# Performance work log

Hardware: AMD Instinct MI355X
Metric: run time of the kernel (lower is better)

The kernel has to match this reference:

```python
import jax, jax.numpy as jnp
import numpy as np

B, T, C, H, WINDOW = 256, 1024, 128, 256, 24


def setup_inputs() -> dict:
    key = jax.random.key(0)
    ks = jax.random.split(key, 9)
    s = 1.0 / np.sqrt(H)  # torch LSTMCell uniform init scale
    return {
        "x": jax.random.normal(ks[0], (B, T, C), dtype=jnp.float32),
        "W_ih": jax.random.uniform(ks[1], (4 * H, C), jnp.float32, -s, s),
        "W_hh": jax.random.uniform(ks[2], (4 * H, H), jnp.float32, -s, s),
        "b_ih": jax.random.uniform(ks[3], (4 * H,), jnp.float32, -s, s),
        "b_hh": jax.random.uniform(ks[4], (4 * H,), jnp.float32, -s, s),
        "W_skip": jax.random.normal(ks[5], (H, H), dtype=jnp.float32) * np.sqrt(2.0 / (H + H)),
        "b_skip": jnp.zeros((H,), jnp.float32),
        "h0": jax.random.normal(ks[6], (1, H), dtype=jnp.float32) * np.sqrt(2.0 / (1 + H)),
        "c0": jax.random.normal(ks[7], (1, H), dtype=jnp.float32) * np.sqrt(2.0 / (1 + H)),
    }


def reference(x, W_ih, W_hh, b_ih, b_hh, W_skip, b_skip, h0, c0):
    Bb, Tt, _ = x.shape
    Hh = h0.shape[1]
    h = jnp.tile(h0, (Bb, 1))
    c = jnp.tile(c0, (Bb, 1))
    # ring buffer of the last WINDOW hidden states (output[i-WINDOW] lives at slot i % WINDOW)
    buf = jnp.zeros((WINDOW, Bb, Hh), x.dtype)
    # precompute the input contribution to the gates for all timesteps: [T, B, 4H]
    xg = jnp.einsum('btc,gc->tbg', x, W_ih) + b_ih + b_hh

    def step(carry, inp):
        h, c, buf = carry
        xg_t, i = inp
        idx = i % WINDOW
        skip = jax.lax.dynamic_index_in_dim(buf, idx, 0, keepdims=False)  # output[i-WINDOW]
        mask = (i >= WINDOW).astype(x.dtype)
        h_in = h + mask * (skip @ W_skip.T + b_skip)
        gates = xg_t + h_in @ W_hh.T  # [B, 4H]
        gi, gf, gg, go = jnp.split(gates, 4, axis=-1)  # torch order: i, f, g, o
        c_new = jax.nn.sigmoid(gf) * c + jax.nn.sigmoid(gi) * jnp.tanh(gg)
        h_new = jax.nn.sigmoid(go) * jnp.tanh(c_new)
        buf = jax.lax.dynamic_update_index_in_dim(buf, h_new, idx, 0)
        return (h_new, c_new, buf), h_new

    (h, c, _), out = jax.lax.scan(step, (h, c, buf), (xg, jnp.arange(Tt)))
    output = jnp.swapaxes(out, 0, 1)  # [B, T, H]
    return output, h, c
```

## Files before the change

### kernel.cpp

```cpp
#include <hip/hip_runtime.h>
#include <cstddef>

#define Bn  256
#define Tn  1024
#define Cn  128
#define Hn  256
#define WIN 24

#define NRG 16
#define NUG 8
#define RPB 16
#define UPB 32

#define AGENT __HIP_MEMORY_SCOPE_AGENT
#define RLX   __ATOMIC_RELAXED

typedef __attribute__((ext_vector_type(8))) short bf16x8;
typedef __attribute__((ext_vector_type(4))) float f32x4;

#define MFMA(a, b, c) __builtin_amdgcn_mfma_f32_16x16x32_bf16((a), (b), (c), 0, 0, 0)

struct __align__(64) Flag { int v; int pad[15]; };
__device__ Flag g_flag[NRG][NUG];
__device__ unsigned short g_hx_hi[2][Bn][Hn];
__device__ unsigned short g_hx_lo[2][Bn][Hn];

__device__ inline unsigned short f2bf(float f) {
    union { float f; unsigned u; } v; v.f = f;
    unsigned r = (v.u + 0x7FFF + ((v.u >> 16) & 1)) >> 16;
    return (unsigned short)r;
}
__device__ inline float bf2f(unsigned short b) {
    union { unsigned u; float f; } v; v.u = (unsigned)b << 16;
    return v.f;
}
__device__ inline void split8(const float* s, bf16x8& hi, bf16x8& lo) {
    #pragma unroll
    for (int e = 0; e < 8; ++e) {
        unsigned short h = f2bf(s[e]);
        float r = s[e] - bf2f(h);
        hi[e] = (short)h;
        lo[e] = (short)f2bf(r);
    }
}
__device__ inline float fsigm(float x) {
    return __builtin_amdgcn_rcpf(1.f + exp2f(x * -1.442695041f));
}
__device__ inline float ftanh(float x) {
    return 1.f - 2.f * __builtin_amdgcn_rcpf(1.f + exp2f(x * 2.885390082f));
}

__global__ __launch_bounds__(256) void init_sync(const float* __restrict__ h0) {
    int i = blockIdx.x * 256 + threadIdx.x;
    int b = i >> 8, u = i & 255;
    float hv = h0[u];
    unsigned short hi = f2bf(hv);
    g_hx_hi[0][b][u] = hi;
    g_hx_lo[0][b][u] = f2bf(hv - bf2f(hi));
    g_hx_hi[1][b][u] = 0;
    g_hx_lo[1][b][u] = 0;
    if (i < NRG * NUG) ((Flag*)g_flag)[i].v = 0;
}

__global__ __launch_bounds__(512, 1) void lstm_persist(
    const float* __restrict__ x,
    const float* __restrict__ W_ih, const float* __restrict__ W_hh,
    const float* __restrict__ b_ih, const float* __restrict__ b_hh,
    const float* __restrict__ W_skip, const float* __restrict__ b_skip,
    const float* __restrict__ h0, const float* __restrict__ c0,
    float* __restrict__ outp, float* __restrict__ hbuf, float* __restrict__ cbuf)
{
    __shared__ bf16x8 s_ga[2][12][64];
    __shared__ bf16x8 s_sa[2][8][64];
    __shared__ float  s_part[8][64][4];
    __shared__ float  s_sk[4][2][64][4];
    __shared__ __align__(16) unsigned short s_hown_hi[16][32];
    __shared__ __align__(16) unsigned short s_hown_lo[16][32];
    __shared__ float  s_hout[16][32];
    __shared__ float  s_bias[128];
    __shared__ float  s_bskip[UPB];
    __shared__ float  s_pad[5000];

    const int tid = threadIdx.x;
    if (tid == 0) ((volatile float*)s_pad)[0] = 0.f;

    const int xcd = blockIdx.x & 7, slot = blockIdx.x >> 3;
    const int rg = (xcd << 1) | (slot >> 3), ug = slot & 7;
    const int row0 = rg * RPB, u0 = ug * UPB;

    const int w = tid >> 6, lane = tid & 63;
    const int g  = w >> 1, uh = w & 1;
    const int nl = lane & 15, kq = lane >> 4;
    const int sm = lane & 15;
    const int k0 = w * 32 + kq * 8;
    const bool own = (w == ug);
    const int cm = tid >> 5, cu = tid & 31;
    const int cli = ((cm >> 2) << 4) | (cu & 15), cr = cm & 3, cuh = cu >> 4;
    const int ksx2 = w - 4;
    const int mx2 = lane & 15, kqx2 = lane >> 4;

    bf16x8 whh_hi[8], whh_lo[8], wx_hi[4], wx_lo[4], ws_hi[2], ws_lo[2];
    {
        const int Rg = g * Hn + u0 + uh * 16 + nl;
        const float* wr = W_hh + (size_t)Rg * Hn;
        #pragma unroll
        for (int j = 0; j < 8; ++j) {
            float tmp[8];
            const int k = j * 32 + kq * 8;
            #pragma unroll
            for (int e = 0; e < 8; ++e) tmp[e] = wr[k + e];
            split8(tmp, whh_hi[j], whh_lo[j]);
        }
        const float* wr2 = W_ih + (size_t)Rg * Cn;
        #pragma unroll
        for (int j = 0; j < 4; ++j) {
            float tmp[8];
            const int k = j * 32 + kq * 8;
            #pragma unroll
            for (int e = 0; e < 8; ++e) tmp[e] = wr2[k + e];
            split8(tmp, wx_hi[j], wx_lo[j]);
        }
        const int Rs = u0 + uh * 16 + nl;
        const float* wr3 = W_skip + (size_t)Rs * Hn;
        #pragma unroll
        for (int j = 0; j < 2; ++j) {
            float tmp[8];
            const int k = ((w >> 1) * 2 + j) * 32 + kq * 8;
            #pragma unroll
            for (int e = 0; e < 8; ++e) tmp[e] = wr3[k + e];
            split8(tmp, ws_hi[j], ws_lo[j]);
        }
    }
    if (tid < 128) s_bias[tid] = b_ih[(tid >> 5) * Hn + u0 + (tid & 31)]
                               + b_hh[(tid >> 5) * Hn + u0 + (tid & 31)];
    if (tid < UPB) s_bskip[tid] = b_skip[u0 + tid];

    float c_reg = c0[u0 + cu];
    {
        float hv = h0[u0 + cu];
        unsigned short phi = f2bf(hv);
        s_hown_hi[cm][cu] = phi;
        s_hown_lo[cm][cu] = f2bf(hv - bf2f(phi));
    }
    if (tid < 256) {
        const int ksx = tid >> 6;
        const float* src = x + (size_t)(row0 + sm) * (Tn * Cn) + ksx * 32 + kq * 8;
        float tmp[8];
        #pragma unroll
        for (int e = 0; e < 8; ++e) tmp[e] = src[e];
        bf16x8 hi, lo; split8(tmp, hi, lo);
        s_ga[0][ksx][lane] = hi; s_ga[1][ksx][lane] = lo;
    }
    f32x4 ring_a = {0.f,0.f,0.f,0.f}, ring_b = {0.f,0.f,0.f,0.f};
    __syncthreads();

    for (int t = 0; t < Tn; ++t) {
        const bool do_ring = (t >= WIN - 1) && (t < Tn - 1);
        const bool nr      = (t >= WIN - 2) && (t < Tn - 2);
        const int  par     = t & 1;

        int fv = 0x7fffffff;
        if (!own) fv = __hip_atomic_load(&g_flag[rg][w].v, RLX, AGENT);

        if (do_ring) {
            asm volatile("s_waitcnt vmcnt(0)" : "+v"(ring_a), "+v"(ring_b) :: "memory");
            float rvv[8];
            #pragma unroll
            for (int e = 0; e < 4; ++e) { rvv[e] = ring_a[e]; rvv[4 + e] = ring_b[e]; }
            bf16x8 hi, lo; split8(rvv, hi, lo);
            s_sa[0][w][lane] = hi; s_sa[1][w][lane] = lo;
        }
        __syncthreads();

        const unsigned short* hip_ = &g_hx_hi[par][row0 + sm][k0];
        const unsigned short* lop_ = &g_hx_lo[par][row0 + sm][k0];
        bf16x8 ha, hb;
        bool have = false;
        if (!own && fv >= t) {
            have = true;
            asm volatile("global_load_dwordx4 %0, %2, off sc0 sc1\n\t"
                         "global_load_dwordx4 %1, %3, off sc0 sc1"
                         : "=&v"(ha), "=&v"(hb) : "v"(hip_), "v"(lop_) : "memory");
        }

        f32x4 ac0 = {0.f,0.f,0.f,0.f}, ac1 = {0.f,0.f,0.f,0.f}, ac2 = {0.f,0.f,0.f,0.f};
        #pragma unroll
        for (int j = 0; j < 4; ++j) {
            bf16x8 ah = s_ga[0][j][lane], al = s_ga[1][j][lane];
            ac0 = MFMA(ah, wx_hi[j], ac0);
            ac1 = MFMA(ah, wx_lo[j], ac1);
            ac2 = MFMA(al, wx_hi[j], ac2);
        }
        if (do_ring) {
            f32x4 sk0 = {0.f,0.f,0.f,0.f}, sk1 = {0.f,0.f,0.f,0.f}, sk2 = {0.f,0.f,0.f,0.f};
            #pragma unroll
            for (int j = 0; j < 2; ++j) {
                const int ks = (w >> 1) * 2 + j;
                bf16x8 ah = s_sa[0][ks][lane], al = s_sa[1][ks][lane];
                sk0 = MFMA(ah, ws_hi[j], sk0);
                sk1 = MFMA(ah, ws_lo[j], sk1);
                sk2 = MFMA(al, ws_hi[j], sk2);
            }
            *(f32x4*)&s_sk[w >> 1][w & 1][lane][0] = sk0 + sk1 + sk2;
        }
        if (!own && !have) {
            fv = __hip_atomic_load(&g_flag[rg][w].v, RLX, AGENT);
            if (fv >= t) {
                have = true;
                asm volatile("global_load_dwordx4 %0, %2, off sc0 sc1\n\t"
                             "global_load_dwordx4 %1, %3, off sc0 sc1"
                             : "=&v"(ha), "=&v"(hb) : "v"(hip_), "v"(lop_) : "memory");
            }
        }

        if (!own) {
            while (fv < t)
                fv = __hip_atomic_load(&g_flag[rg][w].v, RLX, AGENT);
            if (!have) {
                asm volatile("global_load_dwordx4 %0, %2, off sc0 sc1\n\t"
                             "global_load_dwordx4 %1, %3, off sc0 sc1"
                             : "=&v"(ha), "=&v"(hb) : "v"(hip_), "v"(lop_) : "memory");
            }
            asm volatile("s_waitcnt vmcnt(0)" : "+v"(ha), "+v"(hb) :: "memory");
            s_ga[0][4 + w][lane] = ha;
            s_ga[1][4 + w][lane] = hb;
        } else {
            s_ga[0][4 + w][lane] = *(const bf16x8*)&s_hown_hi[sm][kq * 8];
            s_ga[1][4 + w][lane] = *(const bf16x8*)&s_hown_lo[sm][kq * 8];
        }
        f32x4 xa, xb;
        const bool xst = (w >= 4) && (t + 1 < Tn);
        if (xst) {
            const float* xsrc = x + (size_t)(row0 + mx2) * (Tn * Cn)
                                  + (size_t)(t + 1) * Cn + ksx2 * 32 + kqx2 * 8;
            xa = *(const f32x4*)xsrc;
            xb = *(const f32x4*)(xsrc + 4);
        }
        __syncthreads();

        #pragma unroll
        for (int j = 0; j < 8; ++j) {
            bf16x8 ah = s_ga[0][4 + j][lane], al = s_ga[1][4 + j][lane];
            ac0 = MFMA(ah, whh_hi[j], ac0);
            ac1 = MFMA(ah, whh_lo[j], ac1);
            ac2 = MFMA(al, whh_hi[j], ac2);
        }
        *(f32x4*)&s_part[w][lane][0] = ac0 + ac1 + ac2;
        __syncthreads();

        {
            float gv[4];
            #pragma unroll
            for (int g2 = 0; g2 < 4; ++g2)
                gv[g2] = s_part[g2 * 2 + cuh][cli][cr] + s_bias[g2 * 32 + cu];
            float si = fsigm(gv[0]);
            float sf = fsigm(gv[1]);
            float gt = ftanh(gv[2]);
            float so = fsigm(gv[3]);
            c_reg = sf * c_reg + si * gt;
            float hn = so * ftanh(c_reg);
            s_hout[cm][cu] = hn;
            if (t < Tn - 1) {
                float hin = hn;
                if (do_ring) {
                    float sk = s_sk[0][cuh][cli][cr] + s_sk[1][cuh][cli][cr]
                             + s_sk[2][cuh][cli][cr] + s_sk[3][cuh][cli][cr];
                    hin += sk + s_bskip[cu];
                }
                unsigned short phi = f2bf(hin);
                s_hown_hi[cm][cu] = phi;
                s_hown_lo[cm][cu] = f2bf(hin - bf2f(phi));
            } else {
                hbuf[(size_t)(row0 + cm) * Hn + u0 + cu] = hn;
                cbuf[(size_t)(row0 + cm) * Hn + u0 + cu] = c_reg;
            }
        }
        __syncthreads();

        if (tid < 64) {
            if (t < Tn - 1) {
                const int r8 = tid >> 2, q = tid & 3;
                f32x4 v = *(const f32x4*)&s_hown_hi[r8][q * 8];
                unsigned short* dst = &g_hx_hi[par ^ 1][row0 + r8][u0 + q * 8];
                asm volatile("global_store_dwordx4 %0, %1, off sc0 sc1"
                             :: "v"(dst), "v"(v) : "memory");
            }
        } else if (tid < 128) {
            if (t < Tn - 1) {
                const int r8 = (tid - 64) >> 2, q = tid & 3;
                f32x4 v = *(const f32x4*)&s_hown_lo[r8][q * 8];
                unsigned short* dst = &g_hx_lo[par ^ 1][row0 + r8][u0 + q * 8];
                asm volatile("global_store_dwordx4 %0, %1, off sc0 sc1"
                             :: "v"(dst), "v"(v) : "memory");
            }
        } else if (tid < 256) {
            const int i = tid - 128, r8 = i >> 3, q = i & 7;
            f32x4 v = *(const f32x4*)&s_hout[r8][q * 4];
            float* dst = &outp[(size_t)(row0 + r8) * (Tn * Hn) + (size_t)t * Hn + u0 + q * 4];
            asm volatile("global_store_dwordx4 %0, %1, off sc0 sc1"
                         :: "v"(dst), "v"(v) : "memory");
        } else if (xst) {
            float tmp[8];
            #pragma unroll
            for (int e = 0; e < 4; ++e) { tmp[e] = xa[e]; tmp[4 + e] = xb[e]; }
            bf16x8 hi, lo; split8(tmp, hi, lo);
            s_ga[0][ksx2][lane] = hi;
            s_ga[1][ksx2][lane] = lo;
        }

        asm volatile("s_waitcnt vmcnt(0)" ::: "memory");
        __syncthreads();
        if (t < Tn - 1 && tid == 0)
            __hip_atomic_store(&g_flag[rg][ug].v, t + 1, RLX, AGENT);

        if (nr) {
            const float* rsrc = outp + (size_t)(row0 + sm) * (Tn * Hn)
                                     + (size_t)(t - (WIN - 2)) * Hn + k0;
            asm volatile("global_load_dwordx4 %0, %2, off sc0 sc1\n\t"
                         "global_load_dwordx4 %1, %2, off offset:16 sc0 sc1"
                         : "=&v"(ring_a), "=&v"(ring_b) : "v"(rsrc) : "memory");
        }
    }
}

extern "C" void kernel_launch(void* const* d_in, const int* in_sizes, int n_in,
                              void* d_out, int out_size, void* d_ws, size_t ws_size,
                              hipStream_t stream)
{
    const float* x      = (const float*)d_in[0];
    const float* W_ih   = (const float*)d_in[1];
    const float* W_hh   = (const float*)d_in[2];
    const float* b_ih   = (const float*)d_in[3];
    const float* b_hh   = (const float*)d_in[4];
    const float* W_skip = (const float*)d_in[5];
    const float* b_skip = (const float*)d_in[6];
    const float* h0     = (const float*)d_in[7];
    const float* c0     = (const float*)d_in[8];

    float* outp = (float*)d_out;
    float* hbuf = outp + (size_t)Bn * Tn * Hn;
    float* cbuf = hbuf + (size_t)Bn * Hn;

    init_sync<<<256, 256, 0, stream>>>(h0);
    lstm_persist<<<128, 512, 0, stream>>>(x, W_ih, W_hh, b_ih, b_hh,
                                          W_skip, b_skip, h0, c0, outp, hbuf, cbuf);
}
```

Before: 3.184 ms.

## Publish per-wave ready flags and prefetch flag loads to shorten the cross-block handshake

Each producer wave now publishes its own flag (one for the hi half, one for the lo half) right after its stores drain. This replaces the block-wide waitcnt, __syncthreads and single-thread flag store at the end of each step. Consumers prefetch both flags with one dwordx2 load issued at the end of the previous step and take their minimum. The ring-buffer conversion and skip MFMAs move after the W_hh MFMAs, so the per-step critical path through the inter-block dependency gets shorter. The change drops one barrier per step but relies on per-wave waitcnt ordering and relaxed atomics for memory visibility.

```diff
diff --git a/kernel.cpp b/kernel.cpp
--- a/kernel.cpp
+++ b/kernel.cpp
@@ -17,11 +17,12 @@
 
 typedef __attribute__((ext_vector_type(8))) short bf16x8;
 typedef __attribute__((ext_vector_type(4))) float f32x4;
+typedef __attribute__((ext_vector_type(2))) int   i32x2;
 
 #define MFMA(a, b, c) __builtin_amdgcn_mfma_f32_16x16x32_bf16((a), (b), (c), 0, 0, 0)
 
-struct __align__(64) Flag { int v; int pad[15]; };
-__device__ Flag g_flag[NRG][NUG];
+struct __align__(64) Flag2 { int f0; int f1; int pad[14]; };
+__device__ Flag2 g_flag[NRG][NUG];
 __device__ unsigned short g_hx_hi[2][Bn][Hn];
 __device__ unsigned short g_hx_lo[2][Bn][Hn];
 
@@ -59,7 +60,7 @@
     g_hx_lo[0][b][u] = f2bf(hv - bf2f(hi));
     g_hx_hi[1][b][u] = 0;
     g_hx_lo[1][b][u] = 0;
-    if (i < NRG * NUG) ((Flag*)g_flag)[i].v = 0;
+    if (i < NRG * NUG * 16) ((int*)g_flag)[i] = 0;
 }
 
 __global__ __launch_bounds__(512, 1) void lstm_persist(
@@ -152,35 +153,33 @@
         s_ga[0][ksx][lane] = hi; s_ga[1][ksx][lane] = lo;
     }
     f32x4 ring_a = {0.f,0.f,0.f,0.f}, ring_b = {0.f,0.f,0.f,0.f};
-    __syncthreads();
+    i32x2 fs = {0, 0};
+    const int* fp2 = &g_flag[rg][w].f0;
+    if (!own)
+        asm volatile("global_load_dwordx2 %0, %1, off sc0 sc1"
+                     : "=&v"(fs) : "v"(fp2) : "memory");
 
     for (int t = 0; t < Tn; ++t) {
         const bool do_ring = (t >= WIN - 1) && (t < Tn - 1);
         const bool nr      = (t >= WIN - 2) && (t < Tn - 2);
         const int  par     = t & 1;
 
-        int fv = 0x7fffffff;
-        if (!own) fv = __hip_atomic_load(&g_flag[rg][w].v, RLX, AGENT);
-
-        if (do_ring) {
-            asm volatile("s_waitcnt vmcnt(0)" : "+v"(ring_a), "+v"(ring_b) :: "memory");
-            float rvv[8];
-            #pragma unroll
-            for (int e = 0; e < 4; ++e) { rvv[e] = ring_a[e]; rvv[4 + e] = ring_b[e]; }
-            bf16x8 hi, lo; split8(rvv, hi, lo);
-            s_sa[0][w][lane] = hi; s_sa[1][w][lane] = lo;
-        }
         __syncthreads();
 
         const unsigned short* hip_ = &g_hx_hi[par][row0 + sm][k0];
         const unsigned short* lop_ = &g_hx_lo[par][row0 + sm][k0];
         bf16x8 ha, hb;
+        int fv = 0x7fffffff;
         bool have = false;
-        if (!own && fv >= t) {
-            have = true;
-            asm volatile("global_load_dwordx4 %0, %2, off sc0 sc1\n\t"
-                         "global_load_dwordx4 %1, %3, off sc0 sc1"
-                         : "=&v"(ha), "=&v"(hb) : "v"(hip_), "v"(lop_) : "memory");
+        if (!own) {
+            asm volatile("s_waitcnt vmcnt(0)" : "+v"(fs) :: "memory");
+            fv = fs.x < fs.y ? fs.x : fs.y;
+            if (fv >= t) {
+                have = true;
+                asm volatile("global_load_dwordx4 %0, %2, off sc0 sc1\n\t"
+                             "global_load_dwordx4 %1, %3, off sc0 sc1"
+                             : "=&v"(ha), "=&v"(hb) : "v"(hip_), "v"(lop_) : "memory");
+            }
         }
 
         f32x4 ac0 = {0.f,0.f,0.f,0.f}, ac1 = {0.f,0.f,0.f,0.f}, ac2 = {0.f,0.f,0.f,0.f};
@@ -191,20 +190,12 @@
             ac1 = MFMA(ah, wx_lo[j], ac1);
             ac2 = MFMA(al, wx_hi[j], ac2);
         }
-        if (do_ring) {
-            f32x4 sk0 = {0.f,0.f,0.f,0.f}, sk1 = {0.f,0.f,0.f,0.f}, sk2 = {0.f,0.f,0.f,0.f};
-            #pragma unroll
-            for (int j = 0; j < 2; ++j) {
-                const int ks = (w >> 1) * 2 + j;
-                bf16x8 ah = s_sa[0][ks][lane], al = s_sa[1][ks][lane];
-                sk0 = MFMA(ah, ws_hi[j], sk0);
-                sk1 = MFMA(ah, ws_lo[j], sk1);
-                sk2 = MFMA(al, ws_hi[j], sk2);
-            }
-            *(f32x4*)&s_sk[w >> 1][w & 1][lane][0] = sk0 + sk1 + sk2;
-        }
+
         if (!own && !have) {
-            fv = __hip_atomic_load(&g_flag[rg][w].v, RLX, AGENT);
+            asm volatile("global_load_dwordx2 %0, %1, off sc0 sc1\n\t"
+                         "s_waitcnt vmcnt(0)"
+                         : "=&v"(fs) : "v"(fp2) : "memory");
+            fv = fs.x < fs.y ? fs.x : fs.y;
             if (fv >= t) {
                 have = true;
                 asm volatile("global_load_dwordx4 %0, %2, off sc0 sc1\n\t"
@@ -214,19 +205,33 @@
         }
 
         if (!own) {
-            while (fv < t)
-                fv = __hip_atomic_load(&g_flag[rg][w].v, RLX, AGENT);
+            while (fv < t) {
+                asm volatile("global_load_dwordx2 %0, %1, off sc0 sc1\n\t"
+                             "s_waitcnt vmcnt(0)"
+                             : "=&v"(fs) : "v"(fp2) : "memory");
+                fv = fs.x < fs.y ? fs.x : fs.y;
+            }
             if (!have) {
                 asm volatile("global_load_dwordx4 %0, %2, off sc0 sc1\n\t"
                              "global_load_dwordx4 %1, %3, off sc0 sc1"
                              : "=&v"(ha), "=&v"(hb) : "v"(hip_), "v"(lop_) : "memory");
             }
-            asm volatile("s_waitcnt vmcnt(0)" : "+v"(ha), "+v"(hb) :: "memory");
+            asm volatile("s_waitcnt vmcnt(0)"
+                         : "+v"(ha), "+v"(hb), "+v"(ring_a), "+v"(ring_b) :: "memory");
             s_ga[0][4 + w][lane] = ha;
             s_ga[1][4 + w][lane] = hb;
         } else {
+            asm volatile("s_waitcnt vmcnt(0)"
+                         : "+v"(ring_a), "+v"(ring_b) :: "memory");
             s_ga[0][4 + w][lane] = *(const bf16x8*)&s_hown_hi[sm][kq * 8];
             s_ga[1][4 + w][lane] = *(const bf16x8*)&s_hown_lo[sm][kq * 8];
+        }
+        if (do_ring) {
+            float rvv[8];
+            #pragma unroll
+            for (int e = 0; e < 4; ++e) { rvv[e] = ring_a[e]; rvv[4 + e] = ring_b[e]; }
+            bf16x8 hi, lo; split8(rvv, hi, lo);
+            s_sa[0][w][lane] = hi; s_sa[1][w][lane] = lo;
         }
         f32x4 xa, xb;
         const bool xst = (w >= 4) && (t + 1 < Tn);
@@ -244,6 +249,18 @@
             ac0 = MFMA(ah, whh_hi[j], ac0);
             ac1 = MFMA(ah, whh_lo[j], ac1);
             ac2 = MFMA(al, whh_hi[j], ac2);
+        }
+        if (do_ring) {
+            f32x4 sk0 = {0.f,0.f,0.f,0.f}, sk1 = {0.f,0.f,0.f,0.f}, sk2 = {0.f,0.f,0.f,0.f};
+            #pragma unroll
+            for (int j = 0; j < 2; ++j) {
+                const int ks = (w >> 1) * 2 + j;
+                bf16x8 ah = s_sa[0][ks][lane], al = s_sa[1][ks][lane];
+                sk0 = MFMA(ah, ws_hi[j], sk0);
+                sk1 = MFMA(ah, ws_lo[j], sk1);
+                sk2 = MFMA(al, ws_hi[j], sk2);
+            }
+            *(f32x4*)&s_sk[w >> 1][w & 1][lane][0] = sk0 + sk1 + sk2;
         }
         *(f32x4*)&s_part[w][lane][0] = ac0 + ac1 + ac2;
         __syncthreads();
@@ -284,6 +301,9 @@
                 unsigned short* dst = &g_hx_hi[par ^ 1][row0 + r8][u0 + q * 8];
                 asm volatile("global_store_dwordx4 %0, %1, off sc0 sc1"
                              :: "v"(dst), "v"(v) : "memory");
+                asm volatile("s_waitcnt vmcnt(0)" ::: "memory");
+                if (lane == 0)
+                    __hip_atomic_store(&g_flag[rg][ug].f0, t + 1, RLX, AGENT);
             }
         } else if (tid < 128) {
             if (t < Tn - 1) {
@@ -292,6 +312,9 @@
                 unsigned short* dst = &g_hx_lo[par ^ 1][row0 + r8][u0 + q * 8];
                 asm volatile("global_store_dwordx4 %0, %1, off sc0 sc1"
                              :: "v"(dst), "v"(v) : "memory");
+                asm volatile("s_waitcnt vmcnt(0)" ::: "memory");
+                if (lane == 0)
+                    __hip_atomic_store(&g_flag[rg][ug].f1, t + 1, RLX, AGENT);
             }
         } else if (tid < 256) {
             const int i = tid - 128, r8 = i >> 3, q = i & 7;
@@ -308,11 +331,9 @@
             s_ga[1][ksx2][lane] = lo;
         }
 
-        asm volatile("s_waitcnt vmcnt(0)" ::: "memory");
-        __syncthreads();
-        if (t < Tn - 1 && tid == 0)
-            __hip_atomic_store(&g_flag[rg][ug].v, t + 1, RLX, AGENT);
-
+        if (t < Tn - 1 && !own)
+            asm volatile("global_load_dwordx2 %0, %1, off sc0 sc1"
+                         : "=&v"(fs) : "v"(fp2) : "memory");
         if (nr) {
             const float* rsrc = outp + (size_t)(row0 + sm) * (Tn * Hn)
                                      + (size_t)(t - (WIN - 2)) * Hn + k0;
```

Result: slower. 3.688 ms (+15.8%).
